# Performance work log

Measured on AMD Instinct MI355X. Metric: run time of the kernel, lower is better.

Reference implementation:

```python
import jax, jax.numpy as jnp
import numpy as np

KERNEL_CONST = 2.5652997311834374e-21  # constant value filling the depthwise kernel


def setup_inputs() -> dict:
    key = jax.random.key(0)
    H = W = 1024   # arg0_1, arg1_1: output (= input) spatial size
    Kh = Kw = 1024  # arg3_1, arg4_1: kernel spatial size (full-image box kernel)
    x = jax.random.normal(key, (2, 3, H, W), dtype=jnp.float32)
    return {"arg0_1": H, "arg1_1": W, "arg2_1": x, "arg3_1": Kh, "arg4_1": Kw}


def _box_conv(x, H, W, Kh, Kw):
    # reflection pad exactly as the torch graph: left/top = (k-1)//2, right/bottom = k-1-left
    pl = (Kw - 1) // 2
    pr = (Kw - 1) - pl
    pt = (Kh - 1) // 2
    pb = (Kh - 1) - pt
    p = jnp.pad(x, ((0, 0), (0, 0), (pt, pb), (pl, pr)), mode="reflect")
    # depthwise conv with a constant-valued [Kh,Kw] kernel == const * sliding box sum.
    # Computed in O(HW) via an integral image (2D prefix sum) instead of dense conv.
    S = jnp.cumsum(jnp.cumsum(p, axis=-2), axis=-1)
    S = jnp.pad(S, ((0, 0), (0, 0), (1, 0), (1, 0)))  # zero row/col for inclusive sums
    box = (S[..., Kh:Kh + H, Kw:Kw + W]
           - S[..., :H, Kw:Kw + W]
           - S[..., Kh:Kh + H, :W]
           + S[..., :H, :W])
    return jnp.float32(KERNEL_CONST) * box  # shape [2, 3, H, W]


def reference(arg0_1, arg1_1, arg2_1, arg3_1, arg4_1):
    return _box_conv(arg2_1, arg0_1, arg1_1, arg3_1, arg4_1)
```

## Files before the change

### kernel.cpp

```cpp
#include <hip/hip_runtime.h>


static constexpr float KC = 2.5652997311834374e-21f;
#define IMG (1024 * 1024)

__device__ __forceinline__ float hwindow(const float* S, int o) {
    float r = 0.f;
    if (o <= 510) r += S[512 - o] - S[1];
    const int b0 = o > 511 ? o - 511 : 0;
    const int b1 = o + 513 < 1024 ? o + 513 : 1024;
    r += S[b1] - S[b0];
    if (o >= 512) r += S[1023] - S[1534 - o];
    return r;
}

__device__ __forceinline__ void hrow_emit2(float4 u0, float4 u1,
                                           float* S0, float* S1,
                                           float* wt0, float* wt1,
                                           float* orow0, float* orow1, int t) {
    const float a0 = u0.x, a1 = a0 + u0.y, a2 = a1 + u0.z, a3 = a2 + u0.w;
    const float b0 = u1.x, b1 = b0 + u1.y, b2 = b1 + u1.z, b3 = b2 + u1.w;
    const int lane = t & 63, wave = t >> 6;
    float incA = a3, incB = b3;
    #pragma unroll
    for (int off = 1; off < 64; off <<= 1) {
        float nA = __shfl_up(incA, off);
        float nB = __shfl_up(incB, off);
        if (lane >= off) { incA += nA; incB += nB; }
    }
    if (lane == 63) { wt0[wave] = incA; wt1[wave] = incB; }
    __syncthreads();
    float woffA = 0.f, woffB = 0.f;
    for (int w = 0; w < wave; ++w) { woffA += wt0[w]; woffB += wt1[w]; }
    const float exA = woffA + incA - a3;
    const float exB = woffB + incB - b3;
    S0[4 * t + 0] = exA;      S1[4 * t + 0] = exB;
    S0[4 * t + 1] = exA + a0; S1[4 * t + 1] = exB + b0;
    S0[4 * t + 2] = exA + a1; S1[4 * t + 2] = exB + b1;
    S0[4 * t + 3] = exA + a2; S1[4 * t + 3] = exB + b2;
    if (t == 255) { S0[1024] = exA + a3; S1[1024] = exB + b3; }
    __syncthreads();
    #pragma unroll
    for (int m = 0; m < 4; ++m) {
        const int o = t + 256 * m;
        orow0[o] = KC * hwindow(S0, o);
        orow1[o] = KC * hwindow(S1, o);
    }
}

__global__ __launch_bounds__(256) void scanx_kernel(const float* __restrict__ x,
                                                    float* __restrict__ BP) {
    __shared__ float B[257][33];
    const int t = threadIdx.x;
    const int ch = blockIdx.x >> 5, cg = blockIdx.x & 31;
    const int col0 = cg * 32;
    const int c = t & 31, g = t >> 5;
    const float* xc = x + (size_t)ch * IMG + col0 + c;

    #pragma unroll 4
    for (int i = 0; i < 32; ++i) {
        const int band = g + 8 * i;
        const float* p = xc + (size_t)band * 4 * 1024;
        B[band][c] = (p[0] + p[1024]) + (p[2048] + p[3072]);
    }
    __syncthreads();

    const int lane = t & 63, wv = t >> 6;
    #pragma unroll
    for (int i = 0; i < 8; ++i) {
        const int cc = wv * 8 + i;
        float v0 = B[lane][cc], v1 = B[lane + 64][cc],
              v2 = B[lane + 128][cc], v3 = B[lane + 192][cc];
        float i0 = v0, i1 = v1, i2 = v2, i3 = v3;
        #pragma unroll
        for (int off = 1; off < 64; off <<= 1) {
            float n0 = __shfl_up(i0, off), n1 = __shfl_up(i1, off);
            float n2 = __shfl_up(i2, off), n3 = __shfl_up(i3, off);
            if (lane >= off) { i0 += n0; i1 += n1; i2 += n2; i3 += n3; }
        }
        const float t0 = __shfl(i0, 63), t1 = __shfl(i1, 63), t2 = __shfl(i2, 63);
        B[lane][cc]       = i0 - v0;
        B[lane + 64][cc]  = t0 + i1 - v1;
        B[lane + 128][cc] = t0 + t1 + i2 - v2;
        B[lane + 192][cc] = t0 + t1 + t2 + i3 - v3;
        if (lane == 63) B[256][cc] = t0 + t1 + t2 + i3;
    }
    __syncthreads();

    float* Bp = BP + (size_t)ch * 257 * 1024 + col0;
    #pragma unroll
    for (int i = 0; i < 33; ++i) {
        const int idx = i * 256 + t;
        if (idx < 257 * 32) {
            const int k = idx >> 5, cw = idx & 31;
            Bp[(size_t)k * 1024 + cw] = B[k][cw];
        }
    }
}

__global__ __launch_bounds__(256) void vslideh_kernel(const float* __restrict__ x,
                                                      const float* __restrict__ BP,
                                                      float* __restrict__ out) {
    __shared__ float S[2][1025];
    __shared__ float wtot[2][4];
    const int t = threadIdx.x;
    const int ch = blockIdx.x >> 8, band = blockIdx.x & 255;
    const int O = band * 4;
    const float* xc = x + (size_t)ch * IMG;
    const float* Bc = BP + (size_t)ch * 257 * 1024;
    float* oc = out + (size_t)ch * IMG;

    #define LD4(base, row) (reinterpret_cast<const float4*>((base) + (size_t)(row) * 1024)[t])

    float4 u0, u1, u2, u3;
    if (band < 128) {
        const float4 bA = LD4(Bc, (512 - O) >> 2);
        const float4 x0 = LD4(xc, 0);
        const float4 bB = LD4(Bc, (512 + O) >> 2);
        const float4 xb = LD4(xc, O + 512);
        u0.x = bA.x - x0.x + bB.x + xb.x;
        u0.y = bA.y - x0.y + bB.y + xb.y;
        u0.z = bA.z - x0.z + bB.z + xb.z;
        u0.w = bA.w - x0.w + bB.w + xb.w;
        {
            const float4 a = LD4(xc, O + 513), s = LD4(xc, 511 - O);
            u1.x = u0.x + a.x - s.x; u1.y = u0.y + a.y - s.y;
            u1.z = u0.z + a.z - s.z; u1.w = u0.w + a.w - s.w;
        }
        {
            const float4 a = LD4(xc, O + 514), s = LD4(xc, 510 - O);
            u2.x = u1.x + a.x - s.x; u2.y = u1.y + a.y - s.y;
            u2.z = u1.z + a.z - s.z; u2.w = u1.w + a.w - s.w;
        }
        if (band == 127) {
            u3 = LD4(Bc, 256);
        } else {
            const float4 a = LD4(xc, O + 515), s = LD4(xc, 509 - O);
            u3.x = u2.x + a.x - s.x; u3.y = u2.y + a.y - s.y;
            u3.z = u2.z + a.z - s.z; u3.w = u2.w + a.w - s.w;
        }
    } else {
        const float4 bt = LD4(Bc, 256);
        const float4 bA = LD4(Bc, (O - 512) >> 2);
        const float4 xm = LD4(xc, 1023);
        const float4 bB = LD4(Bc, (1536 - O) >> 2);
        const float4 xf = LD4(xc, 1535 - O);
        float4 acc;
        acc.x = bt.x - bA.x + (bt.x - xm.x) - (bB.x - xf.x);
        acc.y = bt.y - bA.y + (bt.y - xm.y) - (bB.y - xf.y);
        acc.z = bt.z - bA.z + (bt.z - xm.z) - (bB.z - xf.z);
        acc.w = bt.w - bA.w + (bt.w - xm.w) - (bB.w - xf.w);
        {
            const float4 a = LD4(xc, 1534 - O), s = LD4(xc, O - 512);
            u0.x = acc.x + a.x - s.x; u0.y = acc.y + a.y - s.y;
            u0.z = acc.z + a.z - s.z; u0.w = acc.w + a.w - s.w;
        }
        {
            const float4 a = LD4(xc, 1533 - O), s = LD4(xc, O - 511);
            u1.x = u0.x + a.x - s.x; u1.y = u0.y + a.y - s.y;
            u1.z = u0.z + a.z - s.z; u1.w = u0.w + a.w - s.w;
        }
        {
            const float4 a = LD4(xc, 1532 - O), s = LD4(xc, O - 510);
            u2.x = u1.x + a.x - s.x; u2.y = u1.y + a.y - s.y;
            u2.z = u1.z + a.z - s.z; u2.w = u1.w + a.w - s.w;
        }
        {
            const float4 a = LD4(xc, 1531 - O), s = LD4(xc, O - 509);
            u3.x = u2.x + a.x - s.x; u3.y = u2.y + a.y - s.y;
            u3.z = u2.z + a.z - s.z; u3.w = u2.w + a.w - s.w;
        }
    }
    #undef LD4

    hrow_emit2(u0, u1, S[0], S[1], wtot[0], wtot[1],
               oc + (size_t)O * 1024, oc + (size_t)(O + 1) * 1024, t);
    hrow_emit2(u2, u3, S[0], S[1], wtot[0], wtot[1],
               oc + (size_t)(O + 2) * 1024, oc + (size_t)(O + 3) * 1024, t);
}

extern "C" void kernel_launch(void* const* d_in, const int* in_sizes, int n_in,
                              void* d_out, int out_size, void* d_ws, size_t ws_size,
                              hipStream_t stream) {
    const float* x = (const float*)d_in[2];
    float* out = (float*)d_out;
    float* BP = (float*)d_ws;
    scanx_kernel<<<192, 256, 0, stream>>>(x, BP);
    vslideh_kernel<<<1536, 256, 0, stream>>>(x, BP, out);
}
```

Before: 33.10 us.

## Vectorize scan loads, widen scan blocks, fuse four-row horizontal emit with float4 stores

The column-band scan kernel now runs 512 threads and loads float4 vectors, which halves per-thread column work and widens global loads. The sliding-window kernel scans all four output rows in one pass, using two barriers instead of four. Each thread then writes four contiguous outputs as a float4 instead of strided scalars. The risks are a larger shared-memory footprint (4x1025 floats), higher register pressure, and stride-4 LDS reads in hwindow that may cause bank conflicts.

```diff
diff --git a/kernel.cpp b/kernel.cpp
--- a/kernel.cpp
+++ b/kernel.cpp
@@ -14,61 +14,32 @@
     return r;
 }
 
-__device__ __forceinline__ void hrow_emit2(float4 u0, float4 u1,
-                                           float* S0, float* S1,
-                                           float* wt0, float* wt1,
-                                           float* orow0, float* orow1, int t) {
-    const float a0 = u0.x, a1 = a0 + u0.y, a2 = a1 + u0.z, a3 = a2 + u0.w;
-    const float b0 = u1.x, b1 = b0 + u1.y, b2 = b1 + u1.z, b3 = b2 + u1.w;
-    const int lane = t & 63, wave = t >> 6;
-    float incA = a3, incB = b3;
-    #pragma unroll
-    for (int off = 1; off < 64; off <<= 1) {
-        float nA = __shfl_up(incA, off);
-        float nB = __shfl_up(incB, off);
-        if (lane >= off) { incA += nA; incB += nB; }
-    }
-    if (lane == 63) { wt0[wave] = incA; wt1[wave] = incB; }
-    __syncthreads();
-    float woffA = 0.f, woffB = 0.f;
-    for (int w = 0; w < wave; ++w) { woffA += wt0[w]; woffB += wt1[w]; }
-    const float exA = woffA + incA - a3;
-    const float exB = woffB + incB - b3;
-    S0[4 * t + 0] = exA;      S1[4 * t + 0] = exB;
-    S0[4 * t + 1] = exA + a0; S1[4 * t + 1] = exB + b0;
-    S0[4 * t + 2] = exA + a1; S1[4 * t + 2] = exB + b1;
-    S0[4 * t + 3] = exA + a2; S1[4 * t + 3] = exB + b2;
-    if (t == 255) { S0[1024] = exA + a3; S1[1024] = exB + b3; }
-    __syncthreads();
-    #pragma unroll
-    for (int m = 0; m < 4; ++m) {
-        const int o = t + 256 * m;
-        orow0[o] = KC * hwindow(S0, o);
-        orow1[o] = KC * hwindow(S1, o);
-    }
-}
-
-__global__ __launch_bounds__(256) void scanx_kernel(const float* __restrict__ x,
+__global__ __launch_bounds__(512) void scanx_kernel(const float* __restrict__ x,
                                                     float* __restrict__ BP) {
     __shared__ float B[257][33];
     const int t = threadIdx.x;
     const int ch = blockIdx.x >> 5, cg = blockIdx.x & 31;
     const int col0 = cg * 32;
-    const int c = t & 31, g = t >> 5;
-    const float* xc = x + (size_t)ch * IMG + col0 + c;
-
-    #pragma unroll 4
-    for (int i = 0; i < 32; ++i) {
-        const int band = g + 8 * i;
-        const float* p = xc + (size_t)band * 4 * 1024;
-        B[band][c] = (p[0] + p[1024]) + (p[2048] + p[3072]);
+    const int c4 = t & 7, g = t >> 3;
+    const float4* xc = reinterpret_cast<const float4*>(x + (size_t)ch * IMG + col0) + c4;
+
+    #pragma unroll
+    for (int i = 0; i < 4; ++i) {
+        const int band = g + 64 * i;
+        const float4* p = xc + (size_t)band * 4 * 256;
+        const float4 r0 = p[0], r1 = p[256], r2 = p[512], r3 = p[768];
+        const int cc = 4 * c4;
+        B[band][cc + 0] = (r0.x + r1.x) + (r2.x + r3.x);
+        B[band][cc + 1] = (r0.y + r1.y) + (r2.y + r3.y);
+        B[band][cc + 2] = (r0.z + r1.z) + (r2.z + r3.z);
+        B[band][cc + 3] = (r0.w + r1.w) + (r2.w + r3.w);
     }
     __syncthreads();
 
     const int lane = t & 63, wv = t >> 6;
     #pragma unroll
-    for (int i = 0; i < 8; ++i) {
-        const int cc = wv * 8 + i;
+    for (int i = 0; i < 4; ++i) {
+        const int cc = wv * 4 + i;
         float v0 = B[lane][cc], v1 = B[lane + 64][cc],
               v2 = B[lane + 128][cc], v3 = B[lane + 192][cc];
         float i0 = v0, i1 = v1, i2 = v2, i3 = v3;
@@ -89,8 +60,8 @@
 
     float* Bp = BP + (size_t)ch * 257 * 1024 + col0;
     #pragma unroll
-    for (int i = 0; i < 33; ++i) {
-        const int idx = i * 256 + t;
+    for (int i = 0; i < 17; ++i) {
+        const int idx = i * 512 + t;
         if (idx < 257 * 32) {
             const int k = idx >> 5, cw = idx & 31;
             Bp[(size_t)k * 1024 + cw] = B[k][cw];
@@ -101,8 +72,8 @@
 __global__ __launch_bounds__(256) void vslideh_kernel(const float* __restrict__ x,
                                                       const float* __restrict__ BP,
                                                       float* __restrict__ out) {
-    __shared__ float S[2][1025];
-    __shared__ float wtot[2][4];
+    __shared__ float S[4][1025];
+    __shared__ float wtot[4][4];
     const int t = threadIdx.x;
     const int ch = blockIdx.x >> 8, band = blockIdx.x & 255;
     const int O = band * 4;
@@ -173,10 +144,58 @@
     }
     #undef LD4
 
-    hrow_emit2(u0, u1, S[0], S[1], wtot[0], wtot[1],
-               oc + (size_t)O * 1024, oc + (size_t)(O + 1) * 1024, t);
-    hrow_emit2(u2, u3, S[0], S[1], wtot[0], wtot[1],
-               oc + (size_t)(O + 2) * 1024, oc + (size_t)(O + 3) * 1024, t);
+    const int lane = t & 63, wave = t >> 6;
+
+    const float a0 = u0.x, a1 = a0 + u0.y, a2 = a1 + u0.z, a3 = a2 + u0.w;
+    const float b0 = u1.x, b1 = b0 + u1.y, b2 = b1 + u1.z, b3 = b2 + u1.w;
+    const float c0 = u2.x, c1 = c0 + u2.y, c2 = c1 + u2.z, c3 = c2 + u2.w;
+    const float d0 = u3.x, d1 = d0 + u3.y, d2 = d1 + u3.z, d3 = d2 + u3.w;
+    float iA = a3, iB = b3, iC = c3, iD = d3;
+    #pragma unroll
+    for (int off = 1; off < 64; off <<= 1) {
+        float nA = __shfl_up(iA, off), nB = __shfl_up(iB, off);
+        float nC = __shfl_up(iC, off), nD = __shfl_up(iD, off);
+        if (lane >= off) { iA += nA; iB += nB; iC += nC; iD += nD; }
+    }
+    if (lane == 63) {
+        wtot[0][wave] = iA; wtot[1][wave] = iB;
+        wtot[2][wave] = iC; wtot[3][wave] = iD;
+    }
+    __syncthreads();
+
+    float wA = 0.f, wB = 0.f, wC = 0.f, wD = 0.f;
+    for (int w = 0; w < wave; ++w) {
+        wA += wtot[0][w]; wB += wtot[1][w];
+        wC += wtot[2][w]; wD += wtot[3][w];
+    }
+    const float eA = wA + iA - a3;
+    const float eB = wB + iB - b3;
+    const float eC = wC + iC - c3;
+    const float eD = wD + iD - d3;
+    S[0][4 * t + 0] = eA;      S[0][4 * t + 1] = eA + a0;
+    S[0][4 * t + 2] = eA + a1; S[0][4 * t + 3] = eA + a2;
+    S[1][4 * t + 0] = eB;      S[1][4 * t + 1] = eB + b0;
+    S[1][4 * t + 2] = eB + b1; S[1][4 * t + 3] = eB + b2;
+    S[2][4 * t + 0] = eC;      S[2][4 * t + 1] = eC + c0;
+    S[2][4 * t + 2] = eC + c1; S[2][4 * t + 3] = eC + c2;
+    S[3][4 * t + 0] = eD;      S[3][4 * t + 1] = eD + d0;
+    S[3][4 * t + 2] = eD + d1; S[3][4 * t + 3] = eD + d2;
+    if (t == 255) {
+        S[0][1024] = eA + a3; S[1][1024] = eB + b3;
+        S[2][1024] = eC + c3; S[3][1024] = eD + d3;
+    }
+    __syncthreads();
+
+    const int ox = 4 * t;
+    #pragma unroll
+    for (int j = 0; j < 4; ++j) {
+        float4 o;
+        o.x = KC * hwindow(S[j], ox + 0);
+        o.y = KC * hwindow(S[j], ox + 1);
+        o.z = KC * hwindow(S[j], ox + 2);
+        o.w = KC * hwindow(S[j], ox + 3);
+        reinterpret_cast<float4*>(oc + (size_t)(O + j) * 1024)[t] = o;
+    }
 }
 
 extern "C" void kernel_launch(void* const* d_in, const int* in_sizes, int n_in,
@@ -185,6 +204,6 @@
     const float* x = (const float*)d_in[2];
     float* out = (float*)d_out;
     float* BP = (float*)d_ws;
-    scanx_kernel<<<192, 256, 0, stream>>>(x, BP);
+    scanx_kernel<<<192, 512, 0, stream>>>(x, BP);
     vslideh_kernel<<<1536, 256, 0, stream>>>(x, BP, out);
 }
```

Measured after the change: 29.53 us. 1.12x faster.
